# Kernel tuning notes

Hardware: AMD Instinct MI355X
Metric: run time of the kernel (lower is better)

Reference implementation:

```python
import jax, jax.numpy as jnp
import numpy as np

DIM = 768
N_HEADS = 12
HEAD_DIM = DIM // N_HEADS
HIDDEN = 4 * DIM
EPS = 1e-5


def _layernorm(x, gamma, beta):
    mu = jnp.mean(x, axis=-1, keepdims=True)
    var = jnp.mean(jnp.square(x - mu), axis=-1, keepdims=True)
    return (x - mu) * jax.lax.rsqrt(var + EPS) * gamma + beta


def setup_inputs() -> dict:
    key = jax.random.key(0)
    ks = jax.random.split(key, 8)
    B, N = 16, 1024
    s = 0.02
    return {
        "x": jax.random.normal(ks[0], (B, N, DIM), jnp.float32),
        "Wqkv": jax.random.normal(ks[1], (DIM, 3 * DIM), jnp.float32) * s,
        "bqkv": jnp.zeros((3 * DIM,), jnp.float32),
        "Wproj": jax.random.normal(ks[2], (DIM, DIM), jnp.float32) * s,
        "bproj": jnp.zeros((DIM,), jnp.float32),
        "g1": jnp.ones((DIM,), jnp.float32),
        "b1": jnp.zeros((DIM,), jnp.float32),
        "g2": jnp.ones((DIM,), jnp.float32),
        "b2": jnp.zeros((DIM,), jnp.float32),
        "W1": jax.random.normal(ks[3], (DIM, HIDDEN), jnp.float32) * s,
        "bf1": jnp.zeros((HIDDEN,), jnp.float32),
        "W2": jax.random.normal(ks[4], (HIDDEN, DIM), jnp.float32) * s,
        "bf2": jnp.zeros((DIM,), jnp.float32),
    }


def reference(x, Wqkv, bqkv, Wproj, bproj, g1, b1, g2, b2, W1, bf1, W2, bf2):
    B, N, _ = x.shape
    # --- attention branch (pre-LN) ---
    h = _layernorm(x, g1, b1)
    qkv = (h @ Wqkv + bqkv).reshape(B, N, 3, N_HEADS, HEAD_DIM)
    qkv = jnp.transpose(qkv, (2, 0, 3, 1, 4))  # [3, B, H, N, D]
    q, k, v = qkv[0], qkv[1], qkv[2]
    # NOTE: source scales by dim**-0.5, not head_dim**-0.5 (faithful)
    scores = jnp.einsum("bhnd,bhmd->bhnm", q, k) * (DIM ** -0.5)
    attn = jax.nn.softmax(scores, axis=-1)
    out = jnp.einsum("bhnm,bhmd->bhnd", attn, v)
    out = jnp.transpose(out, (0, 2, 1, 3)).reshape(B, N, DIM)
    x = x + (out @ Wproj + bproj)
    # --- MLP branch ---
    h2 = _layernorm(x, g2, b2)
    ff = jax.nn.relu(h2 @ W1 + bf1) @ W2 + bf2
    return x + ff
```

## Files before the change

### kernel.cpp

```cpp
#include <hip/hip_runtime.h>
#include <cstdint>
#include <cstddef>

typedef unsigned short u16;
typedef __bf16 bf16x8 __attribute__((ext_vector_type(8)));
typedef unsigned short u16x8 __attribute__((ext_vector_type(8)));
typedef float f32x4 __attribute__((ext_vector_type(4)));

#define DIMN 768
#define BNROWS 16384
#define NH 12
#define HD 64
#define HID 3072
#define QKVN 2304

__device__ __forceinline__ u16 f2bf(float f) {
  unsigned u = __builtin_bit_cast(unsigned, f);
  u += 0x7fffu + ((u >> 16) & 1u);
  return (u16)(u >> 16);
}

__device__ __forceinline__ bf16x8 ld8(const u16* p) {
  u16x8 v = *reinterpret_cast<const u16x8*>(p);
  return __builtin_bit_cast(bf16x8, v);
}

__device__ __forceinline__ void gload16(const void* g, void* l) {
  __builtin_amdgcn_global_load_lds(
      (const __attribute__((address_space(1))) unsigned int*)g,
      (__attribute__((address_space(3))) unsigned int*)l, 16, 0, 0);
}

#define MFMA(a, b, c) __builtin_amdgcn_mfma_f32_16x16x32_bf16(a, b, c, 0, 0, 0)

__global__ __launch_bounds__(256) void twb_k(const float* __restrict__ W,
                                             u16* __restrict__ Wt, int K, int N) {
  __shared__ float tile[32][33];
  const int n0 = blockIdx.x * 32, k0 = blockIdx.y * 32;
  const int tx = threadIdx.x & 31, ty = threadIdx.x >> 5;
#pragma unroll
  for (int i = 0; i < 4; i++)
    tile[ty + i * 8][tx] = W[(size_t)(k0 + ty + i * 8) * N + n0 + tx];
  __syncthreads();
#pragma unroll
  for (int i = 0; i < 4; i++)
    Wt[(size_t)(n0 + ty + i * 8) * K + k0 + tx] = f2bf(tile[tx][ty + i * 8]);
}

__global__ __launch_bounds__(256) void ln_k(const float* __restrict__ x,
                                            const float* __restrict__ g,
                                            const float* __restrict__ bta,
                                            u16* __restrict__ outp) {
  const int row = blockIdx.x * 4 + (threadIdx.x >> 6);
  const int lane = threadIdx.x & 63;
  const float4* xr = (const float4*)(x + (size_t)row * DIMN);
  float4 v[3];
  float s = 0.f, ss = 0.f;
#pragma unroll
  for (int c = 0; c < 3; c++) {
    v[c] = xr[c * 64 + lane];
    s += v[c].x + v[c].y + v[c].z + v[c].w;
    ss += v[c].x * v[c].x + v[c].y * v[c].y + v[c].z * v[c].z + v[c].w * v[c].w;
  }
#pragma unroll
  for (int off = 1; off < 64; off <<= 1) {
    s += __shfl_xor(s, off);
    ss += __shfl_xor(ss, off);
  }
  const float mu = s * (1.f / DIMN);
  const float var = ss * (1.f / DIMN) - mu * mu;
  const float rs = rsqrtf(var + 1e-5f);
  u16* orow = outp + (size_t)row * DIMN;
#pragma unroll
  for (int c = 0; c < 3; c++) {
    float4 gv = ((const float4*)g)[c * 64 + lane];
    float4 bv = ((const float4*)bta)[c * 64 + lane];
    ushort4 o;
    o.x = f2bf((v[c].x - mu) * rs * gv.x + bv.x);
    o.y = f2bf((v[c].y - mu) * rs * gv.y + bv.y);
    o.z = f2bf((v[c].z - mu) * rs * gv.z + bv.z);
    o.w = f2bf((v[c].w - mu) * rs * gv.w + bv.w);
    ((ushort4*)orow)[c * 64 + lane] = o;
  }
}

template <int OUT_BF16, int RELU, int RESID>
__global__ __launch_bounds__(512, 2) void gemm256_k(const u16* __restrict__ A,
                                                    const u16* __restrict__ Bt,
                                                    const float* __restrict__ bias,
                                                    const float* __restrict__ resid,
                                                    void* __restrict__ Cout, int N, int K) {
  __shared__ u16 lds[65536];
  const int tid = threadIdx.x;
  const int m0 = blockIdx.x * 256;
  const int n0 = blockIdx.y * 256;
  const int lane = tid & 63, w = tid >> 6;
  const int wr = w >> 2, wc = w & 3;
  const int lhi = lane >> 4, llo = lane & 15;
  const int rdoff = (lhi ^ ((llo >> 1) & 3)) * 16;
  const int NT = K >> 5;

  const int srow = tid >> 2;
  const int sc8 = ((tid & 3) ^ ((srow >> 1) & 3)) * 8;
  const u16* aS0 = A + (size_t)(m0 + srow) * K + sc8;
  const u16* aS1 = A + (size_t)(m0 + 128 + srow) * K + sc8;
  const u16* bS0 = Bt + (size_t)(n0 + srow) * K + sc8;
  const u16* bS1 = Bt + (size_t)(n0 + 128 + srow) * K + sc8;

  auto slotBase = [&](int t) -> char* { return (char*)lds + ((size_t)(t & 3) << 15); };
  auto stageAB = [&](int t) {
    char* sb = slotBase(t);
    gload16(aS0 + t * 32, sb + tid * 16);
    gload16(aS1 + t * 32, sb + 8192 + tid * 16);
    gload16(bS0 + t * 32, sb + 16384 + tid * 16);
    gload16(bS1 + t * 32, sb + 16384 + 8192 + tid * 16);
  };

  f32x4 acc[8][4] = {};

  stageAB(0);
  stageAB(1);
  stageAB(2);
  asm volatile("s_waitcnt vmcnt(8)" ::: "memory");
  __builtin_amdgcn_s_barrier();

  for (int t = 0; t < NT; ++t) {
    const char* sb = slotBase(t);
    bf16x8 af[8], bfr[4];
#pragma unroll
    for (int ni = 0; ni < 4; ni++)
      bfr[ni] = ld8((const u16*)(sb + 16384 + (wc * 64 + ni * 16 + llo) * 64 + rdoff));
#pragma unroll
    for (int mi = 0; mi < 8; mi++)
      af[mi] = ld8((const u16*)(sb + (wr * 128 + mi * 16 + llo) * 64 + rdoff));
    if (t + 3 < NT) stageAB(t + 3);
    asm volatile("s_waitcnt lgkmcnt(0)" ::: "memory");
    __builtin_amdgcn_sched_barrier(0);
    __builtin_amdgcn_s_setprio(1);
#pragma unroll
    for (int mi = 0; mi < 8; mi++)
#pragma unroll
      for (int ni = 0; ni < 4; ni++) acc[mi][ni] = MFMA(af[mi], bfr[ni], acc[mi][ni]);
    __builtin_amdgcn_s_setprio(0);
    __builtin_amdgcn_sched_barrier(0);
    if (t + 3 < NT) {
      asm volatile("s_waitcnt vmcnt(8)" ::: "memory");
    } else if (t + 2 < NT) {
      asm volatile("s_waitcnt vmcnt(4)" ::: "memory");
    } else if (t + 1 < NT) {
      asm volatile("s_waitcnt vmcnt(0)" ::: "memory");
    }
    __builtin_amdgcn_s_barrier();
  }

#pragma unroll
  for (int mi = 0; mi < 8; mi++)
#pragma unroll
    for (int ni = 0; ni < 4; ni++) {
      const int row = m0 + wr * 128 + mi * 16 + lhi * 4;
      const int col = n0 + wc * 64 + ni * 16 + llo;
      const float bsv = bias[col];
#pragma unroll
      for (int rr = 0; rr < 4; rr++) {
        float v = acc[mi][ni][rr] + bsv;
        if (RELU) v = fmaxf(v, 0.0f);
        const size_t idx = (size_t)(row + rr) * N + col;
        if (RESID) v += resid[idx];
        if (OUT_BF16)
          ((u16*)Cout)[idx] = f2bf(v);
        else
          ((float*)Cout)[idx] = v;
      }
    }
}

template <int OUT_BF16, int RELU, int RESID>
__global__ __launch_bounds__(256, 2) void gemmP_k(const u16* __restrict__ A,
                                                  const u16* __restrict__ Bt,
                                                  const float* __restrict__ bias,
                                                  const float* __restrict__ resid,
                                                  void* __restrict__ Cout, int N, int K) {
  __shared__ u16 lds[3 * 12288];
  const int tid = threadIdx.x;
  const int m0 = blockIdx.x * 256;
  const int n0 = blockIdx.y * 128;
  const int lane = tid & 63, w = tid >> 6;
  const int wr = w >> 1, wc = w & 1;
  const int lhi = lane >> 4, llo = lane & 15;
  const int rdoff = (lhi ^ ((llo >> 1) & 3)) * 16;
  const int NT = K >> 5;

  const int crow = tid >> 2;
  const int kc8 = ((tid & 3) ^ ((crow >> 1) & 3)) * 8;
  const u16* aS = A + (size_t)(m0 + crow) * K + kc8;
  const u16* bS = Bt + (size_t)(n0 + crow) * K + kc8;
  const size_t a64 = (size_t)64 * K;

  auto slotBase = [&](int t) -> char* { return (char*)lds + (t % 3) * 24576; };
  auto stageAll = [&](int t) {
    char* sb = slotBase(t);
    gload16(aS + t * 32, sb + tid * 16);
    gload16(aS + a64 + t * 32, sb + 4096 + tid * 16);
    gload16(aS + 2 * a64 + t * 32, sb + 8192 + tid * 16);
    gload16(aS + 3 * a64 + t * 32, sb + 12288 + tid * 16);
    gload16(bS + t * 32, sb + 16384 + tid * 16);
    gload16(bS + a64 + t * 32, sb + 16384 + 4096 + tid * 16);
  };

  f32x4 acc[8][4] = {};

  stageAll(0);
  stageAll(1);
  asm volatile("s_waitcnt vmcnt(6)" ::: "memory");
  __builtin_amdgcn_s_barrier();

  for (int t = 0; t < NT; ++t) {
    const char* sb = slotBase(t);
    bf16x8 af[8], bfr[4];
#pragma unroll
    for (int ni = 0; ni < 4; ni++)
      bfr[ni] = ld8((const u16*)(sb + 16384 + (wc * 64 + ni * 16 + llo) * 64 + rdoff));
#pragma unroll
    for (int mi = 0; mi < 8; mi++)
      af[mi] = ld8((const u16*)(sb + (wr * 128 + mi * 16 + llo) * 64 + rdoff));
    if (t + 2 < NT) stageAll(t + 2);
    asm volatile("s_waitcnt lgkmcnt(0)" ::: "memory");
    __builtin_amdgcn_sched_barrier(0);
    __builtin_amdgcn_s_setprio(1);
#pragma unroll
    for (int mi = 0; mi < 8; mi++)
#pragma unroll
      for (int ni = 0; ni < 4; ni++) acc[mi][ni] = MFMA(af[mi], bfr[ni], acc[mi][ni]);
    __builtin_amdgcn_s_setprio(0);
    __builtin_amdgcn_sched_barrier(0);
    if (t + 2 < NT) {
      asm volatile("s_waitcnt vmcnt(6)" ::: "memory");
    } else if (t + 1 < NT) {
      asm volatile("s_waitcnt vmcnt(0)" ::: "memory");
    }
    __builtin_amdgcn_s_barrier();
  }

#pragma unroll
  for (int mi = 0; mi < 8; mi++)
#pragma unroll
    for (int ni = 0; ni < 4; ni++) {
      const int row = m0 + wr * 128 + mi * 16 + lhi * 4;
      const int col = n0 + wc * 64 + ni * 16 + llo;
      const float bsv = bias[col];
#pragma unroll
      for (int rr = 0; rr < 4; rr++) {
        float v = acc[mi][ni][rr] + bsv;
        if (RELU) v = fmaxf(v, 0.0f);
        const size_t idx = (size_t)(row + rr) * N + col;
        if (RESID) v += resid[idx];
        if (OUT_BF16)
          ((u16*)Cout)[idx] = f2bf(v);
        else
          ((float*)Cout)[idx] = v;
      }
    }
}

__device__ __forceinline__ bf16x8 ldscale8(const u16* p, float c) {
  u16x8 v = *reinterpret_cast<const u16x8*>(p);
  bf16x8 r;
#pragma unroll
  for (int j = 0; j < 8; j++) {
    float f = __builtin_bit_cast(float, (unsigned)v[j] << 16) * c;
    r[j] = (__bf16)f;
  }
  return r;
}

__device__ __forceinline__ unsigned pack_bf2(float a, float b) {
  unsigned ua = (unsigned)__builtin_bit_cast(u16, (__bf16)a);
  unsigned ub = (unsigned)__builtin_bit_cast(u16, (__bf16)b);
  return ua | (ub << 16);
}

__global__ __launch_bounds__(256) void attn_k(const u16* __restrict__ qkv,
                                              u16* __restrict__ outp) {
  __shared__ u16 Ks[2][64 * 64];
  __shared__ u16 Vt[2][64 * 64];
  __shared__ u16 Ps[4][32 * 64];

  const int tid = threadIdx.x;
  const int f = blockIdx.x;
  const int bh = (f & 7) | ((f >> 6) << 3);
  const int qt = (f >> 3) & 7;
  const int b = bh / NH, h = bh - b * NH;
  const int lane = tid & 63, w = tid >> 6;
  const int lhi = lane >> 4, llo = lane & 15;
  const size_t rowb = (size_t)b * 1024;
  const int wq0 = qt * 128 + w * 32;
  const float SC = 0.052059750f;

  bf16x8 qb[2][2];
#pragma unroll
  for (int mi = 0; mi < 2; mi++) {
    const u16* qrow = qkv + (rowb + wq0 + mi * 16 + llo) * QKVN + h * HD;
    qb[mi][0] = ldscale8(qrow + lhi * 8, SC);
    qb[mi][1] = ldscale8(qrow + 32 + lhi * 8, SC);
  }

  const u16* kbase = qkv + rowb * QKVN + DIMN + h * HD;
  const u16* vbase = qkv + rowb * QKVN + 2 * DIMN + h * HD;
  const int vc8 = w * 8;
  const int sw = (llo & 7) * 8;
  const int rsw = llo & 7;

  const int srow = tid >> 3, su = tid & 7;
  const u16* ksrc = kbase + (size_t)srow * QKVN + (su ^ (srow & 7)) * 8;

  auto stageK = [&](int kt, int buf) {
    const u16* s0 = ksrc + (size_t)kt * 64 * QKVN;
    gload16(s0, (char*)&Ks[buf][0] + tid * 16);
    gload16(s0 + (size_t)32 * QKVN, (char*)&Ks[buf][0] + 4096 + tid * 16);
  };
  auto loadV = [&](int kt, u16x8& a, u16x8& c) {
    const u16* vr = vbase + (size_t)(kt * 64 + lane) * QKVN + vc8;
    a = *reinterpret_cast<const u16x8*>(vr);
    c = *reinterpret_cast<const u16x8*>(vr + 32);
  };
  auto writeV = [&](int buf, u16x8 a, u16x8 c) {
#pragma unroll
    for (int j = 0; j < 8; j++) {
      Vt[buf][(vc8 + j) * 64 + (lane ^ (j * 8))] = a[j];
      Vt[buf][(vc8 + 32 + j) * 64 + (lane ^ (j * 8))] = c[j];
    }
  };

  u16x8 v0, v1, nv0, nv1;

  stageK(0, 0);
  loadV(0, v0, v1);
  stageK(1, 1);
  asm volatile("s_waitcnt vmcnt(2)" ::: "memory");
  writeV(0, v0, v1);
  asm volatile("s_waitcnt lgkmcnt(0)" ::: "memory");
  __builtin_amdgcn_s_barrier();
  __builtin_amdgcn_sched_barrier(0);

  float psum[2] = {0.f, 0.f};
  f32x4 oacc[2][4] = {};

  for (int t = 0; t < 16; t++) {
    if (t < 15) loadV(t + 1, nv0, nv1);

    const u16* kB = &Ks[t & 1][0];
    f32x4 sacc[4][2] = {};
#pragma unroll
    for (int ks = 0; ks < 2; ks++)
#pragma unroll
      for (int ni = 0; ni < 4; ni++) {
        bf16x8 kf = ld8(&kB[(ni * 16 + llo) * 64 + (((ks * 4 + lhi) ^ rsw) * 8)]);
#pragma unroll
        for (int mi = 0; mi < 2; mi++) sacc[ni][mi] = MFMA(kf, qb[mi][ks], sacc[ni][mi]);
      }

    asm volatile("s_waitcnt lgkmcnt(0)" ::: "memory");
    __builtin_amdgcn_s_barrier();
    __builtin_amdgcn_sched_barrier(0);
    if (t + 2 < 16) stageK(t + 2, t & 1);

#pragma unroll
    for (int mi = 0; mi < 2; mi++)
#pragma unroll
      for (int ni = 0; ni < 4; ni++) {
        float p0 = __builtin_amdgcn_exp2f(sacc[ni][mi][0]);
        float p1 = __builtin_amdgcn_exp2f(sacc[ni][mi][1]);
        float p2 = __builtin_amdgcn_exp2f(sacc[ni][mi][2]);
        float p3 = __builtin_amdgcn_exp2f(sacc[ni][mi][3]);
        psum[mi] += (p0 + p1) + (p2 + p3);
        u16* pp = &Ps[w][(mi * 16 + llo) * 64 + ((ni * 16 + lhi * 4) ^ sw)];
        uint2 pw;
        pw.x = pack_bf2(p0, p1);
        pw.y = pack_bf2(p2, p3);
        *reinterpret_cast<uint2*>(pp) = pw;
      }

#pragma unroll
    for (int ks = 0; ks < 2; ks++) {
      const int koff = ks * 32 + lhi * 8;
      bf16x8 pa0 = ld8(&Ps[w][llo * 64 + (koff ^ sw)]);
      bf16x8 pa1 = ld8(&Ps[w][(16 + llo) * 64 + (koff ^ sw)]);
#pragma unroll
      for (int ni = 0; ni < 4; ni++) {
        bf16x8 vb = ld8(&Vt[t & 1][(ni * 16 + llo) * 64 + (koff ^ sw)]);
        oacc[0][ni] = MFMA(pa0, vb, oacc[0][ni]);
        oacc[1][ni] = MFMA(pa1, vb, oacc[1][ni]);
      }
    }

    if (t < 15) {
      if (t + 2 < 16) {
        asm volatile("s_waitcnt vmcnt(2)" ::: "memory");
      } else {
        asm volatile("s_waitcnt vmcnt(0)" ::: "memory");
      }
      writeV((t + 1) & 1, nv0, nv1);
      v0 = nv0; v1 = nv1;
      asm volatile("s_waitcnt lgkmcnt(0)" ::: "memory");
      __builtin_amdgcn_s_barrier();
      __builtin_amdgcn_sched_barrier(0);
    }
  }

  float rl[2][4];
#pragma unroll
  for (int mi = 0; mi < 2; mi++) {
    psum[mi] += __shfl_xor(psum[mi], 16);
    psum[mi] += __shfl_xor(psum[mi], 32);
#pragma unroll
    for (int r = 0; r < 4; r++) rl[mi][r] = 1.0f / __shfl(psum[mi], lhi * 4 + r);
  }

#pragma unroll
  for (int mi = 0; mi < 2; mi++)
#pragma unroll
    for (int ni = 0; ni < 4; ni++)
#pragma unroll
      for (int r = 0; r < 4; r++) {
        const size_t row = rowb + wq0 + mi * 16 + lhi * 4 + r;
        outp[row * DIMN + h * HD + ni * 16 + llo] = f2bf(oacc[mi][ni][r] * rl[mi][r]);
      }
}

extern "C" void kernel_launch(void* const* d_in, const int* in_sizes, int n_in,
                              void* d_out, int out_size, void* d_ws, size_t ws_size,
                              hipStream_t stream) {
  const float* x = (const float*)d_in[0];
  const float* Wqkv = (const float*)d_in[1];
  const float* bqkv = (const float*)d_in[2];
  const float* Wproj = (const float*)d_in[3];
  const float* bproj = (const float*)d_in[4];
  const float* g1 = (const float*)d_in[5];
  const float* b1 = (const float*)d_in[6];
  const float* g2 = (const float*)d_in[7];
  const float* b2 = (const float*)d_in[8];
  const float* W1 = (const float*)d_in[9];
  const float* bf1 = (const float*)d_in[10];
  const float* W2 = (const float*)d_in[11];
  const float* bf2 = (const float*)d_in[12];
  float* outp = (float*)d_out;

  char* p = (char*)d_ws;
  u16* WqkvT = (u16*)p; p += (size_t)QKVN * DIMN * 2;
  u16* WprojT = (u16*)p; p += (size_t)DIMN * DIMN * 2;
  u16* W1T = (u16*)p; p += (size_t)HID * DIMN * 2;
  u16* W2T = (u16*)p; p += (size_t)DIMN * HID * 2;
  u16* bufX = (u16*)p; p += (size_t)BNROWS * DIMN * 2;
  u16* big = (u16*)p; p += (size_t)BNROWS * HID * 2;

  twb_k<<<dim3(QKVN / 32, DIMN / 32), 256, 0, stream>>>(Wqkv, WqkvT, DIMN, QKVN);
  twb_k<<<dim3(DIMN / 32, DIMN / 32), 256, 0, stream>>>(Wproj, WprojT, DIMN, DIMN);
  twb_k<<<dim3(HID / 32, DIMN / 32), 256, 0, stream>>>(W1, W1T, DIMN, HID);
  twb_k<<<dim3(DIMN / 32, HID / 32), 256, 0, stream>>>(W2, W2T, HID, DIMN);

  ln_k<<<BNROWS / 4, 256, 0, stream>>>(x, g1, b1, bufX);
  gemm256_k<1, 0, 0><<<dim3(64, QKVN / 256), 512, 0, stream>>>(bufX, WqkvT, bqkv, nullptr,
                                                               big, QKVN, DIMN);
  attn_k<<<1536, 256, 0, stream>>>(big, bufX);
  gemmP_k<0, 0, 1><<<dim3(64, DIMN / 128), 256, 0, stream>>>(bufX, WprojT, bproj, x, outp,
                                                             DIMN, DIMN);
  ln_k<<<BNROWS / 4, 256, 0, stream>>>(outp, g2, b2, bufX);
  gemm256_k<1, 1, 0><<<dim3(64, HID / 256), 512, 0, stream>>>(bufX, W1T, bf1, nullptr, big,
                                                              HID, DIMN);
  gemmP_k<0, 0, 1><<<dim3(64, DIMN / 128), 256, 0, stream>>>(big, W2T, bf2, outp, outp,
                                                             DIMN, HID);
}
```

Measured before the change: 442.8 us.

## Double-buffer LDS fragment registers and deepen gemmP global prefetch to four stages

```diff
diff --git a/kernel.cpp b/kernel.cpp
--- a/kernel.cpp
+++ b/kernel.cpp
@@ -107,9 +107,9 @@
   const u16* bS0 = Bt + (size_t)(n0 + srow) * K + sc8;
   const u16* bS1 = Bt + (size_t)(n0 + 128 + srow) * K + sc8;
 
-  auto slotBase = [&](int t) -> char* { return (char*)lds + ((size_t)(t & 3) << 15); };
+  auto slotBase = [&](int t) -> const char* { return (const char*)lds + ((size_t)(t & 3) << 15); };
   auto stageAB = [&](int t) {
-    char* sb = slotBase(t);
+    char* sb = (char*)lds + ((size_t)(t & 3) << 15);
     gload16(aS0 + t * 32, sb + tid * 16);
     gload16(aS1 + t * 32, sb + 8192 + tid * 16);
     gload16(bS0 + t * 32, sb + 16384 + tid * 16);
@@ -117,40 +117,52 @@
   };
 
   f32x4 acc[8][4] = {};
+  bf16x8 afc[8], bfc[4], afn[8], bfn[4];
 
   stageAB(0);
   stageAB(1);
   stageAB(2);
-  asm volatile("s_waitcnt vmcnt(8)" ::: "memory");
+  asm volatile("s_waitcnt vmcnt(4)" ::: "memory");
   __builtin_amdgcn_s_barrier();
+  {
+    const char* sb = slotBase(0);
+#pragma unroll
+    for (int ni = 0; ni < 4; ni++)
+      bfc[ni] = ld8((const u16*)(sb + 16384 + (wc * 64 + ni * 16 + llo) * 64 + rdoff));
+#pragma unroll
+    for (int mi = 0; mi < 8; mi++)
+      afc[mi] = ld8((const u16*)(sb + (wr * 128 + mi * 16 + llo) * 64 + rdoff));
+  }
+  asm volatile("s_waitcnt lgkmcnt(0)" ::: "memory");
+  __builtin_amdgcn_sched_barrier(0);
 
   for (int t = 0; t < NT; ++t) {
-    const char* sb = slotBase(t);
-    bf16x8 af[8], bfr[4];
-#pragma unroll
-    for (int ni = 0; ni < 4; ni++)
-      bfr[ni] = ld8((const u16*)(sb + 16384 + (wc * 64 + ni * 16 + llo) * 64 + rdoff));
+    if (t + 3 < NT) stageAB(t + 3);
+    if (t + 1 < NT) {
+      const char* sb = slotBase(t + 1);
+#pragma unroll
+      for (int ni = 0; ni < 4; ni++)
+        bfn[ni] = ld8((const u16*)(sb + 16384 + (wc * 64 + ni * 16 + llo) * 64 + rdoff));
+#pragma unroll
+      for (int mi = 0; mi < 8; mi++)
+        afn[mi] = ld8((const u16*)(sb + (wr * 128 + mi * 16 + llo) * 64 + rdoff));
+    }
 #pragma unroll
     for (int mi = 0; mi < 8; mi++)
-      af[mi] = ld8((const u16*)(sb + (wr * 128 + mi * 16 + llo) * 64 + rdoff));
-    if (t + 3 < NT) stageAB(t + 3);
+#pragma unroll
+      for (int ni = 0; ni < 4; ni++) acc[mi][ni] = MFMA(afc[mi], bfc[ni], acc[mi][ni]);
     asm volatile("s_waitcnt lgkmcnt(0)" ::: "memory");
     __builtin_amdgcn_sched_barrier(0);
-    __builtin_amdgcn_s_setprio(1);
-#pragma unroll
-    for (int mi = 0; mi < 8; mi++)
-#pragma unroll
-      for (int ni = 0; ni < 4; ni++) acc[mi][ni] = MFMA(af[mi], bfr[ni], acc[mi][ni]);
-    __builtin_amdgcn_s_setprio(0);
-    __builtin_amdgcn_sched_barrier(0);
     if (t + 3 < NT) {
-      asm volatile("s_waitcnt vmcnt(8)" ::: "memory");
+      asm volatile("s_waitcnt vmcnt(4)" ::: "memory");
     } else if (t + 2 < NT) {
-      asm volatile("s_waitcnt vmcnt(4)" ::: "memory");
-    } else if (t + 1 < NT) {
       asm volatile("s_waitcnt vmcnt(0)" ::: "memory");
     }
     __builtin_amdgcn_s_barrier();
+#pragma unroll
+    for (int mi = 0; mi < 8; mi++) afc[mi] = afn[mi];
+#pragma unroll
+    for (int ni = 0; ni < 4; ni++) bfc[ni] = bfn[ni];
   }
 
 #pragma unroll
@@ -180,7 +192,7 @@
                                                   const float* __restrict__ bias,
                                                   const float* __restrict__ resid,
                                                   void* __restrict__ Cout, int N, int K) {
-  __shared__ u16 lds[3 * 12288];
+  __shared__ u16 lds[4 * 12288];
   const int tid = threadIdx.x;
   const int m0 = blockIdx.x * 256;
   const int n0 = blockIdx.y * 128;
@@ -196,9 +208,9 @@
   const u16* bS = Bt + (size_t)(n0 + crow) * K + kc8;
   const size_t a64 = (size_t)64 * K;
 
-  auto slotBase = [&](int t) -> char* { return (char*)lds + (t % 3) * 24576; };
+  auto slotBase = [&](int t) -> const char* { return (const char*)lds + (size_t)(t & 3) * 24576; };
   auto stageAll = [&](int t) {
-    char* sb = slotBase(t);
+    char* sb = (char*)lds + (size_t)(t & 3) * 24576;
     gload16(aS + t * 32, sb + tid * 16);
     gload16(aS + a64 + t * 32, sb + 4096 + tid * 16);
     gload16(aS + 2 * a64 + t * 32, sb + 8192 + tid * 16);
@@ -208,37 +220,52 @@
   };
 
   f32x4 acc[8][4] = {};
+  bf16x8 afc[8], bfc[4], afn[8], bfn[4];
 
   stageAll(0);
   stageAll(1);
+  stageAll(2);
   asm volatile("s_waitcnt vmcnt(6)" ::: "memory");
   __builtin_amdgcn_s_barrier();
+  {
+    const char* sb = slotBase(0);
+#pragma unroll
+    for (int ni = 0; ni < 4; ni++)
+      bfc[ni] = ld8((const u16*)(sb + 16384 + (wc * 64 + ni * 16 + llo) * 64 + rdoff));
+#pragma unroll
+    for (int mi = 0; mi < 8; mi++)
+      afc[mi] = ld8((const u16*)(sb + (wr * 128 + mi * 16 + llo) * 64 + rdoff));
+  }
+  asm volatile("s_waitcnt lgkmcnt(0)" ::: "memory");
+  __builtin_amdgcn_sched_barrier(0);
 
   for (int t = 0; t < NT; ++t) {
-    const char* sb = slotBase(t);
-    bf16x8 af[8], bfr[4];
-#pragma unroll
-    for (int ni = 0; ni < 4; ni++)
-      bfr[ni] = ld8((const u16*)(sb + 16384 + (wc * 64 + ni * 16 + llo) * 64 + rdoff));
+    if (t + 3 < NT) stageAll(t + 3);
+    if (t + 1 < NT) {
+      const char* sb = slotBase(t + 1);
+#pragma unroll
+      for (int ni = 0; ni < 4; ni++)
+        bfn[ni] = ld8((const u16*)(sb + 16384 + (wc * 64 + ni * 16 + llo) * 64 + rdoff));
+#pragma unroll
+      for (int mi = 0; mi < 8; mi++)
+        afn[mi] = ld8((const u16*)(sb + (wr * 128 + mi * 16 + llo) * 64 + rdoff));
+    }
 #pragma unroll
     for (int mi = 0; mi < 8; mi++)
-      af[mi] = ld8((const u16*)(sb + (wr * 128 + mi * 16 + llo) * 64 + rdoff));
-    if (t + 2 < NT) stageAll(t + 2);
+#pragma unroll
+      for (int ni = 0; ni < 4; ni++) acc[mi][ni] = MFMA(afc[mi], bfc[ni], acc[mi][ni]);
     asm volatile("s_waitcnt lgkmcnt(0)" ::: "memory");
     __builtin_amdgcn_sched_barrier(0);
-    __builtin_amdgcn_s_setprio(1);
-#pragma unroll
-    for (int mi = 0; mi < 8; mi++)
-#pragma unroll
-      for (int ni = 0; ni < 4; ni++) acc[mi][ni] = MFMA(af[mi], bfr[ni], acc[mi][ni]);
-    __builtin_amdgcn_s_setprio(0);
-    __builtin_amdgcn_sched_barrier(0);
-    if (t + 2 < NT) {
+    if (t + 3 < NT) {
       asm volatile("s_waitcnt vmcnt(6)" ::: "memory");
-    } else if (t + 1 < NT) {
+    } else if (t + 2 < NT) {
       asm volatile("s_waitcnt vmcnt(0)" ::: "memory");
     }
     __builtin_amdgcn_s_barrier();
+#pragma unroll
+    for (int mi = 0; mi < 8; mi++) afc[mi] = afn[mi];
+#pragma unroll
+    for (int ni = 0; ni < 4; ni++) bfc[ni] = bfn[ni];
   }
 
 #pragma unroll
```

Measured after the change: 488.0 us. +10.2%, slower.

## Split GEMM main loop into two phases with register double-buffered LDS fragments

Applied to the files above, without the earlier changes.

```diff
diff --git a/kernel.cpp b/kernel.cpp
--- a/kernel.cpp
+++ b/kernel.cpp
@@ -107,51 +107,94 @@
   const u16* bS0 = Bt + (size_t)(n0 + srow) * K + sc8;
   const u16* bS1 = Bt + (size_t)(n0 + 128 + srow) * K + sc8;
 
-  auto slotBase = [&](int t) -> char* { return (char*)lds + ((size_t)(t & 3) << 15); };
-  auto stageAB = [&](int t) {
-    char* sb = slotBase(t);
+  auto slotBase = [&](int t) -> const char* { return (const char*)lds + ((size_t)(t & 3) << 15); };
+  auto stageA = [&](int t) {
+    char* sb = (char*)lds + ((size_t)(t & 3) << 15);
     gload16(aS0 + t * 32, sb + tid * 16);
     gload16(aS1 + t * 32, sb + 8192 + tid * 16);
-    gload16(bS0 + t * 32, sb + 16384 + tid * 16);
-    gload16(bS1 + t * 32, sb + 16384 + 8192 + tid * 16);
+  };
+  auto stageB = [&](int t) {
+    char* sb = (char*)lds + ((size_t)(t & 3) << 15) + 16384;
+    gload16(bS0 + t * 32, sb + tid * 16);
+    gload16(bS1 + t * 32, sb + 8192 + tid * 16);
   };
 
   f32x4 acc[8][4] = {};
-
-  stageAB(0);
-  stageAB(1);
-  stageAB(2);
+  bf16x8 a03[2][4], bfr[2][4], a47[4];
+
+  stageB(0); stageA(0);
+  stageB(1); stageA(1);
+  stageB(2); stageA(2);
   asm volatile("s_waitcnt vmcnt(8)" ::: "memory");
   __builtin_amdgcn_s_barrier();
-
-  for (int t = 0; t < NT; ++t) {
-    const char* sb = slotBase(t);
-    bf16x8 af[8], bfr[4];
+  {
+    const char* sb = slotBase(0);
 #pragma unroll
     for (int ni = 0; ni < 4; ni++)
-      bfr[ni] = ld8((const u16*)(sb + 16384 + (wc * 64 + ni * 16 + llo) * 64 + rdoff));
-#pragma unroll
-    for (int mi = 0; mi < 8; mi++)
-      af[mi] = ld8((const u16*)(sb + (wr * 128 + mi * 16 + llo) * 64 + rdoff));
-    if (t + 3 < NT) stageAB(t + 3);
-    asm volatile("s_waitcnt lgkmcnt(0)" ::: "memory");
-    __builtin_amdgcn_sched_barrier(0);
-    __builtin_amdgcn_s_setprio(1);
-#pragma unroll
-    for (int mi = 0; mi < 8; mi++)
-#pragma unroll
-      for (int ni = 0; ni < 4; ni++) acc[mi][ni] = MFMA(af[mi], bfr[ni], acc[mi][ni]);
-    __builtin_amdgcn_s_setprio(0);
-    __builtin_amdgcn_sched_barrier(0);
-    if (t + 3 < NT) {
-      asm volatile("s_waitcnt vmcnt(8)" ::: "memory");
-    } else if (t + 2 < NT) {
-      asm volatile("s_waitcnt vmcnt(4)" ::: "memory");
-    } else if (t + 1 < NT) {
-      asm volatile("s_waitcnt vmcnt(0)" ::: "memory");
-    }
-    __builtin_amdgcn_s_barrier();
-  }
+      bfr[0][ni] = ld8((const u16*)(sb + 16384 + (wc * 64 + ni * 16 + llo) * 64 + rdoff));
+#pragma unroll
+    for (int mi = 0; mi < 4; mi++)
+      a03[0][mi] = ld8((const u16*)(sb + (wr * 128 + mi * 16 + llo) * 64 + rdoff));
+  }
+
+#define G256_P1(T, CUR)                                                                  \
+  {                                                                                      \
+    const char* sbp = slotBase(T);                                                       \
+    _Pragma("unroll") for (int mi = 0; mi < 4; mi++)                                     \
+        a47[mi] = ld8((const u16*)(sbp + (wr * 128 + (4 + mi) * 16 + llo) * 64 + rdoff));\
+    if ((T) + 3 < NT) stageB((T) + 3);                                                   \
+    if ((T) + 3 < NT) {                                                                  \
+      asm volatile("s_waitcnt vmcnt(6)" ::: "memory");                                   \
+    } else if ((T) + 2 < NT) {                                                           \
+      asm volatile("s_waitcnt vmcnt(4)" ::: "memory");                                   \
+    } else if ((T) + 1 < NT) {                                                           \
+      asm volatile("s_waitcnt vmcnt(0)" ::: "memory");                                   \
+    }                                                                                    \
+    __builtin_amdgcn_s_barrier();                                                        \
+    asm volatile("s_waitcnt lgkmcnt(4)" ::: "memory");                                   \
+    __builtin_amdgcn_sched_barrier(0);                                                   \
+    __builtin_amdgcn_s_setprio(1);                                                       \
+    _Pragma("unroll") for (int mi = 0; mi < 4; mi++)                                     \
+        _Pragma("unroll") for (int ni = 0; ni < 4; ni++)                                 \
+            acc[mi][ni] = MFMA(a03[CUR][mi], bfr[CUR][ni], acc[mi][ni]);                 \
+    __builtin_amdgcn_s_setprio(0);                                                       \
+    __builtin_amdgcn_sched_barrier(0);                                                   \
+  }
+
+#define G256_P2(T, CUR, NXT)                                                             \
+  {                                                                                      \
+    if ((T) + 1 < NT) {                                                                  \
+      const char* sbn = slotBase((T) + 1);                                               \
+      _Pragma("unroll") for (int ni = 0; ni < 4; ni++)                                   \
+          bfr[NXT][ni] =                                                                 \
+              ld8((const u16*)(sbn + 16384 + (wc * 64 + ni * 16 + llo) * 64 + rdoff));   \
+      _Pragma("unroll") for (int mi = 0; mi < 4; mi++)                                   \
+          a03[NXT][mi] = ld8((const u16*)(sbn + (wr * 128 + mi * 16 + llo) * 64 + rdoff));\
+    }                                                                                    \
+    if ((T) + 3 < NT) stageA((T) + 3);                                                   \
+    __builtin_amdgcn_s_barrier();                                                        \
+    if ((T) + 1 < NT) {                                                                  \
+      asm volatile("s_waitcnt lgkmcnt(8)" ::: "memory");                                 \
+    } else {                                                                             \
+      asm volatile("s_waitcnt lgkmcnt(0)" ::: "memory");                                 \
+    }                                                                                    \
+    __builtin_amdgcn_sched_barrier(0);                                                   \
+    __builtin_amdgcn_s_setprio(1);                                                       \
+    _Pragma("unroll") for (int mi = 0; mi < 4; mi++)                                     \
+        _Pragma("unroll") for (int ni = 0; ni < 4; ni++)                                 \
+            acc[4 + mi][ni] = MFMA(a47[mi], bfr[CUR][ni], acc[4 + mi][ni]);              \
+    __builtin_amdgcn_s_setprio(0);                                                       \
+    __builtin_amdgcn_sched_barrier(0);                                                   \
+  }
+
+  for (int t = 0; t < NT; t += 2) {
+    G256_P1(t, 0)
+    G256_P2(t, 0, 1)
+    G256_P1(t + 1, 1)
+    G256_P2(t + 1, 1, 0)
+  }
+#undef G256_P1
+#undef G256_P2
 
 #pragma unroll
   for (int mi = 0; mi < 8; mi++)
@@ -196,50 +239,93 @@
   const u16* bS = Bt + (size_t)(n0 + crow) * K + kc8;
   const size_t a64 = (size_t)64 * K;
 
-  auto slotBase = [&](int t) -> char* { return (char*)lds + (t % 3) * 24576; };
-  auto stageAll = [&](int t) {
-    char* sb = slotBase(t);
+  auto slotBase = [&](int t) -> const char* { return (const char*)lds + (size_t)(t % 3) * 24576; };
+  auto stage1 = [&](int t) {
+    char* sb = (char*)lds + (size_t)(t % 3) * 24576;
     gload16(aS + t * 32, sb + tid * 16);
     gload16(aS + a64 + t * 32, sb + 4096 + tid * 16);
+    gload16(bS + t * 32, sb + 16384 + tid * 16);
+  };
+  auto stage2 = [&](int t) {
+    char* sb = (char*)lds + (size_t)(t % 3) * 24576;
     gload16(aS + 2 * a64 + t * 32, sb + 8192 + tid * 16);
     gload16(aS + 3 * a64 + t * 32, sb + 12288 + tid * 16);
-    gload16(bS + t * 32, sb + 16384 + tid * 16);
     gload16(bS + a64 + t * 32, sb + 16384 + 4096 + tid * 16);
   };
 
   f32x4 acc[8][4] = {};
-
-  stageAll(0);
-  stageAll(1);
+  bf16x8 a03[2][4], bfr[2][4], a47[4];
+
+  stage1(0); stage2(0);
+  stage1(1); stage2(1);
   asm volatile("s_waitcnt vmcnt(6)" ::: "memory");
   __builtin_amdgcn_s_barrier();
-
-  for (int t = 0; t < NT; ++t) {
-    const char* sb = slotBase(t);
-    bf16x8 af[8], bfr[4];
+  {
+    const char* sb = slotBase(0);
 #pragma unroll
     for (int ni = 0; ni < 4; ni++)
-      bfr[ni] = ld8((const u16*)(sb + 16384 + (wc * 64 + ni * 16 + llo) * 64 + rdoff));
-#pragma unroll
-    for (int mi = 0; mi < 8; mi++)
-      af[mi] = ld8((const u16*)(sb + (wr * 128 + mi * 16 + llo) * 64 + rdoff));
-    if (t + 2 < NT) stageAll(t + 2);
-    asm volatile("s_waitcnt lgkmcnt(0)" ::: "memory");
-    __builtin_amdgcn_sched_barrier(0);
-    __builtin_amdgcn_s_setprio(1);
-#pragma unroll
-    for (int mi = 0; mi < 8; mi++)
-#pragma unroll
-      for (int ni = 0; ni < 4; ni++) acc[mi][ni] = MFMA(af[mi], bfr[ni], acc[mi][ni]);
-    __builtin_amdgcn_s_setprio(0);
-    __builtin_amdgcn_sched_barrier(0);
-    if (t + 2 < NT) {
-      asm volatile("s_waitcnt vmcnt(6)" ::: "memory");
-    } else if (t + 1 < NT) {
-      asm volatile("s_waitcnt vmcnt(0)" ::: "memory");
-    }
-    __builtin_amdgcn_s_barrier();
-  }
+      bfr[0][ni] = ld8((const u16*)(sb + 16384 + (wc * 64 + ni * 16 + llo) * 64 + rdoff));
+#pragma unroll
+    for (int mi = 0; mi < 4; mi++)
+      a03[0][mi] = ld8((const u16*)(sb + (wr * 128 + mi * 16 + llo) * 64 + rdoff));
+  }
+
+#define GP_P1(T, CUR)                                                                    \
+  {                                                                                      \
+    const char* sbp = slotBase(T);                                                       \
+    _Pragma("unroll") for (int mi = 0; mi < 4; mi++)                                     \
+        a47[mi] = ld8((const u16*)(sbp + (wr * 128 + (4 + mi) * 16 + llo) * 64 + rdoff));\
+    if ((T) + 2 < NT) stage1((T) + 2);                                                   \
+    if ((T) + 2 < NT) {                                                                  \
+      asm volatile("s_waitcnt vmcnt(3)" ::: "memory");                                   \
+    } else if ((T) + 1 < NT) {                                                           \
+      asm volatile("s_waitcnt vmcnt(0)" ::: "memory");                                   \
+    }                                                                                    \
+    __builtin_amdgcn_s_barrier();                                                        \
+    asm volatile("s_waitcnt lgkmcnt(4)" ::: "memory");                                   \
+    __builtin_amdgcn_sched_barrier(0);                                                   \
+    __builtin_amdgcn_s_setprio(1);                                                       \
+    _Pragma("unroll") for (int mi = 0; mi < 4; mi++)                                     \
+        _Pragma("unroll") for (int ni = 0; ni < 4; ni++)                                 \
+            acc[mi][ni] = MFMA(a03[CUR][mi], bfr[CUR][ni], acc[mi][ni]);                 \
+    __builtin_amdgcn_s_setprio(0);                                                       \
+    __builtin_amdgcn_sched_barrier(0);                                                   \
+  }
+
+#define GP_P2(T, CUR, NXT)                                                               \
+  {                                                                                      \
+    if ((T) + 1 < NT) {                                                                  \
+      const char* sbn = slotBase((T) + 1);                                               \
+      _Pragma("unroll") for (int ni = 0; ni < 4; ni++)                                   \
+          bfr[NXT][ni] =                                                                 \
+              ld8((const u16*)(sbn + 16384 + (wc * 64 + ni * 16 + llo) * 64 + rdoff));   \
+      _Pragma("unroll") for (int mi = 0; mi < 4; mi++)                                   \
+          a03[NXT][mi] = ld8((const u16*)(sbn + (wr * 128 + mi * 16 + llo) * 64 + rdoff));\
+    }                                                                                    \
+    if ((T) + 2 < NT) stage2((T) + 2);                                                   \
+    __builtin_amdgcn_s_barrier();                                                        \
+    if ((T) + 1 < NT) {                                                                  \
+      asm volatile("s_waitcnt lgkmcnt(8)" ::: "memory");                                 \
+    } else {                                                                             \
+      asm volatile("s_waitcnt lgkmcnt(0)" ::: "memory");                                 \
+    }                                                                                    \
+    __builtin_amdgcn_sched_barrier(0);                                                   \
+    __builtin_amdgcn_s_setprio(1);                                                       \
+    _Pragma("unroll") for (int mi = 0; mi < 4; mi++)                                     \
+        _Pragma("unroll") for (int ni = 0; ni < 4; ni++)                                 \
+            acc[4 + mi][ni] = MFMA(a47[mi], bfr[CUR][ni], acc[4 + mi][ni]);              \
+    __builtin_amdgcn_s_setprio(0);                                                       \
+    __builtin_amdgcn_sched_barrier(0);                                                   \
+  }
+
+  for (int t = 0; t < NT; t += 2) {
+    GP_P1(t, 0)
+    GP_P2(t, 0, 1)
+    GP_P1(t + 1, 1)
+    GP_P2(t + 1, 1, 0)
+  }
+#undef GP_P1
+#undef GP_P2
 
 #pragma unroll
   for (int mi = 0; mi < 8; mi++)
```

Measured after the change: 438.3 us. No clear change (-1.0%).
